# Performance work log

Measured on AMD Instinct MI355X. Metric: run time of the kernel, lower is better.

The kernel has to match this reference:

```python
import jax, jax.numpy as jnp
import numpy as np

B, S, D = 16, 8192, 256
CHUNK_RATIO = 4
EPS = 1e-8  # torch F.cosine_similarity default eps


def setup_inputs() -> dict:
    key = jax.random.key(0)
    ks = jax.random.split(key, 9)
    s = 1.0 / np.sqrt(D).astype(np.float32)
    return {
        "x": jax.random.normal(ks[0], (B, S, D), jnp.float32),
        "Wq": jax.random.normal(ks[1], (D, D), jnp.float32) * s,
        "bq": jax.random.normal(ks[2], (D,), jnp.float32) * s,
        "Wk": jax.random.normal(ks[3], (D, D), jnp.float32) * s,
        "bk": jax.random.normal(ks[4], (D,), jnp.float32) * s,
        "w_vol": jax.random.normal(ks[5], (D,), jnp.float32) * s,
        "b_vol": jax.random.normal(ks[6], (1,), jnp.float32) * s,
        "w_volu": jax.random.normal(ks[7], (D,), jnp.float32) * s,
        "b_volu": jax.random.normal(ks[8], (1,), jnp.float32) * s,
    }


def reference(x, Wq, bq, Wk, bk, w_vol, b_vol, w_volu, b_volu):
    Bn, Sn, Dn = x.shape
    q = x @ Wq + bq                       # (B,S,D)
    k = x @ Wk + bk                       # (B,S,D)
    qs, kx = q[:, 1:], k[:, :-1]          # (B,S-1,D)
    dot = jnp.sum(qs * kx, axis=-1)
    sim = dot / (jnp.maximum(jnp.linalg.norm(qs, axis=-1), EPS)
                 * jnp.maximum(jnp.linalg.norm(kx, axis=-1), EPS))
    boundary_scores = 1.0 - sim           # (B,S-1)
    vol = jax.nn.sigmoid(x @ w_vol + b_vol[0])     # (B,S)
    volu = jax.nn.sigmoid(x @ w_volu + b_volu[0])  # (B,S)
    combined = jnp.concatenate(
        [jnp.ones((Bn, 1), x.dtype),
         boundary_scores + 0.3 * vol[:, 1:] + 0.2 * volu[:, 1:]], axis=1)
    boundary_probs = jax.nn.sigmoid(combined)      # (B,S)
    hard = (boundary_probs > 0.5).astype(x.dtype)  # first pos always 1 (sigmoid(1)>0.5)
    boundaries = hard + boundary_probs - jax.lax.stop_gradient(boundary_probs)
    target = jnp.asarray(Sn / CHUNK_RATIO, x.dtype)
    ratio_loss = (boundaries.sum(axis=1).mean() - target) ** 2
    # vectorized compaction: gather boundary rows to the front, zero-pad to S
    idx = jnp.cumsum(hard.astype(jnp.int32), axis=1) - 1  # destination slot per row
    brow = jnp.arange(Bn)[:, None]
    compressed = jnp.zeros((Bn, Sn, Dn), x.dtype).at[brow, idx].add(x * hard[..., None])
    return compressed, boundary_probs, ratio_loss
```

## Files before the change

kernel.cpp:

```cpp
#include <hip/hip_runtime.h>
#include <math.h>

#define BN 16
#define SN 8192
#define DN 256
#define MBLK 128
#define EPSF 1e-8f

#define CHUNK_B 16384
#define NCHUNK 17
#define LDS_BYTES (3 * CHUNK_B)

typedef __attribute__((ext_vector_type(8))) short short8;
typedef __attribute__((ext_vector_type(4))) float f32x4;

typedef const __attribute__((address_space(1))) unsigned int g_u32;
typedef __attribute__((address_space(3))) unsigned int l_u32;

__device__ __forceinline__ unsigned short f2bf(float f) {
    union { float f; unsigned int u; } cv; cv.f = f;
    unsigned int u = cv.u + 0x7FFFu + ((cv.u >> 16) & 1u);
    return (unsigned short)(u >> 16);
}

__device__ __forceinline__ void gload_lds16(const void* g, void* l) {
    __builtin_amdgcn_global_load_lds((g_u32*)g, (l_u32*)l, 16, 0, 0);
}

__global__ void k0_prep(const float* __restrict__ Wq, const float* __restrict__ Wk,
                        const float* __restrict__ w_vol, const float* __restrict__ w_volu,
                        unsigned char* __restrict__ Wfrag)
{
    const int tid = threadIdx.x;
    const int n   = blockIdx.x * 8 + (tid >> 5);
    const int k8  = tid & 31;
    const int ch  = n >> 4;
    const int cc  = n & 15;
    const int ks  = k8 >> 2;
    const int g   = k8 & 3;

    short8 vq, vk;
    #pragma unroll
    for (int e = 0; e < 8; ++e) {
        const int k = k8 * 8 + e;
        vq[e] = (short)f2bf(Wq[(size_t)k * DN + n]);
        vk[e] = (short)f2bf(Wk[(size_t)k * DN + n]);
    }
    const size_t base = (size_t)ch * CHUNK_B + (size_t)((g * 16 + cc) * 16);
    *(short8*)(Wfrag + base + (size_t)(ks)     * 1024) = vq;
    *(short8*)(Wfrag + base + (size_t)(8 + ks) * 1024) = vk;

    unsigned char* Gfrag = Wfrag + (size_t)16 * CHUNK_B;
    if (blockIdx.x < 2) {
        const int gc = blockIdx.x * 8 + (tid >> 5);
        short8 vg;
        #pragma unroll
        for (int e = 0; e < 8; ++e) {
            const int k = k8 * 8 + e;
            float v = (gc == 0) ? w_vol[k] : ((gc == 1) ? w_volu[k] : 0.0f);
            vg[e] = (short)f2bf(v);
        }
        *(short8*)(Gfrag + (size_t)ks * 1024 + (size_t)((g * 16 + gc) * 16)) = vg;
    } else if (blockIdx.x < 4) {
        short8 z = (short8)(0);
        *(short8*)(Gfrag + 8192 + (size_t)(blockIdx.x - 2) * 4096 + (size_t)tid * 16) = z;
    }
}

__global__ void k0b_kpatch(const float* __restrict__ x, const float* __restrict__ Wk,
                           float* __restrict__ kpatch)
{
    __shared__ float xr[8][DN];
    const int b  = blockIdx.y;
    const int r0 = blockIdx.x * 8;
    const int t  = threadIdx.x;
    #pragma unroll
    for (int m = 0; m < 8; ++m)
        xr[m][t] = x[((size_t)b * SN + 31 + (size_t)(r0 + m) * 32) * DN + t];
    __syncthreads();
    float acc[8];
    #pragma unroll
    for (int m = 0; m < 8; ++m) acc[m] = 0.f;
    #pragma unroll 4
    for (int k = 0; k < DN; ++k) {
        const float w = Wk[(size_t)k * DN + t];
        #pragma unroll
        for (int m = 0; m < 8; ++m) acc[m] = fmaf(xr[m][k], w, acc[m]);
    }
    #pragma unroll
    for (int m = 0; m < 8; ++m)
        kpatch[((size_t)b * 256 + r0 + m) * DN + t] = acc[m];
}

__global__ __launch_bounds__(256, 3) void k1_mfma(
    const float* __restrict__ x,
    const unsigned char* __restrict__ Wfrag,
    const float* __restrict__ kpatch,
    const float* __restrict__ bq, const float* __restrict__ bk,
    const float* __restrict__ b_vol, const float* __restrict__ b_volu,
    float* __restrict__ bp_out, int* __restrict__ flags)
{
    extern __shared__ unsigned char lds[];

    const int tid  = threadIdx.x;
    const int wq   = tid >> 6;
    const int l    = tid & 63;
    const int g    = l >> 4;
    const int c    = l & 15;
    const int b    = blockIdx.y;
    const int blkx = blockIdx.x;
    const int s0   = blkx * MBLK;

    const float* xb = x + (size_t)b * SN * DN;

    {
        unsigned char* reg = lds;
        #pragma unroll
        for (int it = 0; it < 4; ++it) {
            const int f = it * 256 + tid;
            const int rho = f >> 5, ch = f & 31;
            const float4* p = (const float4*)(xb + (size_t)(s0 + rho) * DN + ch * 8);
            const float4 aa = p[0], dd = p[1];
            short8 sv;
            sv[0] = (short)f2bf(aa.x); sv[1] = (short)f2bf(aa.y);
            sv[2] = (short)f2bf(aa.z); sv[3] = (short)f2bf(aa.w);
            sv[4] = (short)f2bf(dd.x); sv[5] = (short)f2bf(dd.y);
            sv[6] = (short)f2bf(dd.z); sv[7] = (short)f2bf(dd.w);
            *(short8*)(reg + rho * 512 + ((ch * 16) ^ ((rho & 7) << 4))) = sv;
        }
    }
    __syncthreads();

    short8 a[2][8];
    #pragma unroll
    for (int qt = 0; qt < 4; ++qt) {
        if (qt < 3) {
            unsigned char* reg = lds + ((qt + 1) & 1) * CHUNK_B;
            #pragma unroll
            for (int it = 0; it < 4; ++it) {
                const int f = it * 256 + tid;
                const int rho = f >> 5, ch = f & 31;
                const float4* p = (const float4*)(xb + (size_t)(s0 + (qt + 1) * 32 + rho) * DN + ch * 8);
                const float4 aa = p[0], dd = p[1];
                short8 sv;
                sv[0] = (short)f2bf(aa.x); sv[1] = (short)f2bf(aa.y);
                sv[2] = (short)f2bf(aa.z); sv[3] = (short)f2bf(aa.w);
                sv[4] = (short)f2bf(dd.x); sv[5] = (short)f2bf(dd.y);
                sv[6] = (short)f2bf(dd.z); sv[7] = (short)f2bf(dd.w);
                *(short8*)(reg + rho * 512 + ((ch * 16) ^ ((rho & 7) << 4))) = sv;
            }
        }
        if (wq == qt) {
            const unsigned char* reg = lds + (qt & 1) * CHUNK_B;
            #pragma unroll
            for (int m = 0; m < 2; ++m) {
                const int rho = m * 16 + c;
                #pragma unroll
                for (int ks = 0; ks < 8; ++ks)
                    a[m][ks] = *(const short8*)(reg + rho * 512 + (((ks * 64) + g * 16) ^ ((rho & 7) << 4)));
            }
        }
        __syncthreads();
    }

    #pragma unroll
    for (int j = 0; j < 4; ++j)
        gload_lds16(Wfrag + j * 4096 + tid * 16, lds + j * 4096 + wq * 1024);
    #pragma unroll
    for (int j = 0; j < 4; ++j)
        gload_lds16(Wfrag + CHUNK_B + j * 4096 + tid * 16, lds + CHUNK_B + j * 4096 + wq * 1024);
    asm volatile("s_waitcnt vmcnt(4)" ::: "memory");
    __builtin_amdgcn_s_barrier();

    float dt[2][4], nqv[2][4], nkv[2][4];
    #pragma unroll
    for (int m = 0; m < 2; ++m)
        #pragma unroll
        for (int r = 0; r < 4; ++r) { dt[m][r] = 0.f; nqv[m][r] = 0.f; nkv[m][r] = 0.f; }
    f32x4 cg0 = (f32x4)(0.f), cg1 = (f32x4)(0.f);

    int kpidx = 4 * blkx + wq - 1;
    if (kpidx < 0) kpidx = 0;
    const float* kpp = kpatch + ((size_t)b * 256 + kpidx) * DN;

    #pragma unroll
    for (int i = 0; i < NCHUNK; ++i) {
        if (i + 2 < NCHUNK) {
            const unsigned char* src = Wfrag + (size_t)(i + 2) * CHUNK_B;
            unsigned char* dst = lds + ((i + 2) % 3) * CHUNK_B;
            #pragma unroll
            for (int j = 0; j < 4; ++j)
                gload_lds16(src + j * 4096 + tid * 16, dst + j * 4096 + wq * 1024);
        }
        const unsigned char* bb = lds + (i % 3) * CHUNK_B;

        if (i < 16) {
            f32x4 cq0 = (f32x4)(0.f), cq1 = (f32x4)(0.f);
            f32x4 ck0 = (f32x4)(0.f), ck1 = (f32x4)(0.f);
            #pragma unroll
            for (int ks = 0; ks < 8; ++ks) {
                const short8 bqf = *(const short8*)(bb + ks * 1024 + l * 16);
                const short8 bkf = *(const short8*)(bb + (8 + ks) * 1024 + l * 16);
                cq0 = __builtin_amdgcn_mfma_f32_16x16x32_bf16(a[0][ks], bqf, cq0, 0, 0, 0);
                cq1 = __builtin_amdgcn_mfma_f32_16x16x32_bf16(a[1][ks], bqf, cq1, 0, 0, 0);
                ck0 = __builtin_amdgcn_mfma_f32_16x16x32_bf16(a[0][ks], bkf, ck0, 0, 0, 0);
                ck1 = __builtin_amdgcn_mfma_f32_16x16x32_bf16(a[1][ks], bkf, ck1, 0, 0, 0);
            }
            const float bqc = bq[i * 16 + c];
            const float bkc = bk[i * 16 + c];
            const float kb  = kpp[i * 16 + c];
            const float sh0 = __shfl(ck0[3], (l - 16) & 63);
            const float sh1 = __shfl(ck1[3], (l - 16) & 63);
            const float cr  = __shfl(ck0[3], 48 + c);
            const float km00 = (g == 0) ? kb : sh0;
            const float km10 = (g == 0) ? cr : sh1;
            const float kv0[4] = {km00, ck0[0], ck0[1], ck0[2]};
            const float kv1[4] = {km10, ck1[0], ck1[1], ck1[2]};
            #pragma unroll
            for (int r = 0; r < 4; ++r) {
                float qv = cq0[r] + bqc;
                float kv = kv0[r] + bkc;
                dt[0][r]  = fmaf(qv, kv, dt[0][r]);
                nqv[0][r] = fmaf(qv, qv, nqv[0][r]);
                nkv[0][r] = fmaf(kv, kv, nkv[0][r]);
                qv = cq1[r] + bqc;
                kv = kv1[r] + bkc;
                dt[1][r]  = fmaf(qv, kv, dt[1][r]);
                nqv[1][r] = fmaf(qv, qv, nqv[1][r]);
                nkv[1][r] = fmaf(kv, kv, nkv[1][r]);
            }
        } else {
            #pragma unroll
            for (int ks = 0; ks < 8; ++ks) {
                const short8 bgf = *(const short8*)(bb + ks * 1024 + l * 16);
                cg0 = __builtin_amdgcn_mfma_f32_16x16x32_bf16(a[0][ks], bgf, cg0, 0, 0, 0);
                cg1 = __builtin_amdgcn_mfma_f32_16x16x32_bf16(a[1][ks], bgf, cg1, 0, 0, 0);
            }
        }

        if (i < NCHUNK - 2) asm volatile("s_waitcnt vmcnt(4)" ::: "memory");
        else                asm volatile("s_waitcnt vmcnt(0)" ::: "memory");
        __builtin_amdgcn_s_barrier();
    }

    #pragma unroll
    for (int m = 0; m < 2; ++m)
        #pragma unroll
        for (int r = 0; r < 4; ++r) {
            float aa = dt[m][r], e = nqv[m][r], f = nkv[m][r];
            #pragma unroll
            for (int mask = 1; mask < 16; mask <<= 1) {
                aa += __shfl_xor(aa, mask);
                e  += __shfl_xor(e, mask);
                f  += __shfl_xor(f, mask);
            }
            dt[m][r] = aa; nqv[m][r] = e; nkv[m][r] = f;
        }
    float vu0[4], vu1[4];
    #pragma unroll
    for (int r = 0; r < 4; ++r) { vu0[r] = __shfl_xor(cg0[r], 1); vu1[r] = __shfl_xor(cg1[r], 1); }

    if (c == 0) {
        const float bv = b_vol[0], bu = b_volu[0];
        #pragma unroll
        for (int m = 0; m < 2; ++m)
            #pragma unroll
            for (int r = 0; r < 4; ++r) {
                const int s = s0 + wq * 32 + m * 16 + g * 4 + r;
                const float cgv = (m == 0) ? cg0[r] : cg1[r];
                const float vuv = (m == 0) ? vu0[r] : vu1[r];
                float comb;
                if (s == 0) comb = 1.0f;
                else {
                    float denom = fmaxf(sqrtf(nqv[m][r]), EPSF) * fmaxf(sqrtf(nkv[m][r]), EPSF);
                    float sim   = dt[m][r] / denom;
                    float vol   = 1.f / (1.f + expf(-(cgv + bv)));
                    float volu  = 1.f / (1.f + expf(-(vuv + bu)));
                    comb = (1.f - sim) + 0.3f * vol + 0.2f * volu;
                }
                const float pbp = 1.f / (1.f + expf(-comb));
                const size_t o = (size_t)b * SN + s;
                bp_out[o] = pbp;
                flags[o]  = (pbp > 0.5f) ? 1 : 0;
            }
    }
}

__global__ void k2_scan(const int* __restrict__ flags,
                        const float* __restrict__ bp,
                        int* __restrict__ pidx,
                        int* __restrict__ cnt,
                        float* __restrict__ bsum)
{
    const int b = blockIdx.x;
    const int t = threadIdx.x;
    __shared__ int   ssum[256];
    __shared__ float sf[256];

    const size_t base = (size_t)b * SN + (size_t)t * 32;
    int f[32];
    int run = 0;
    float fs = 0.f;
    #pragma unroll
    for (int i = 0; i < 32; ++i) {
        f[i] = flags[base + i];
        run += f[i];
        float p  = bp[base + i];
        float hf = (float)f[i];
        fs += hf + p - p;
    }
    ssum[t] = run;
    sf[t]   = fs;
    __syncthreads();

    for (int off = 1; off < 256; off <<= 1) {
        int v = (t >= off) ? ssum[t - off] : 0;
        __syncthreads();
        ssum[t] += v;
        __syncthreads();
    }
    const int incl = ssum[t];
    int running = incl - run;
    #pragma unroll
    for (int i = 0; i < 32; ++i) {
        running += f[i];
        pidx[base + i] = f[i] ? (running - 1) : -1;
    }
    if (t == 255) cnt[b] = incl;

    for (int off = 128; off > 0; off >>= 1) {
        if (t < off) sf[t] += sf[t + off];
        __syncthreads();
    }
    if (t == 0) bsum[b] = sf[0];
}

__global__ void k3_scatter(const float* __restrict__ x,
                           const int* __restrict__ pidx,
                           float* __restrict__ out_comp)
{
    const int row  = blockIdx.x * 4 + (threadIdx.x >> 6);
    const int lane = threadIdx.x & 63;
    const int p = pidx[row];
    if (p < 0) return;
    const int b = row >> 13;
    const float4* src = (const float4*)(x + (size_t)row * DN);
    float4* dst = (float4*)(out_comp + ((size_t)b * SN + p) * DN);
    dst[lane] = src[lane];
}

__global__ void k3b_zerotail(float* __restrict__ out_comp,
                             const int* __restrict__ cnt)
{
    const int gid = blockIdx.x * blockDim.x + threadIdx.x;
    const int b = gid >> 13;
    const int j = gid & (SN - 1);
    if (j >= cnt[b]) {
        float4* dst = (float4*)(out_comp + ((size_t)b * SN + j) * DN);
        const float4 z = make_float4(0.f, 0.f, 0.f, 0.f);
        for (int i = 0; i < DN / 4; ++i) dst[i] = z;
    }
}

__global__ void k4_loss(const float* __restrict__ bsum, float* __restrict__ out_rl)
{
    if (threadIdx.x == 0) {
        float acc = 0.f;
        for (int i = 0; i < BN; ++i) acc += bsum[i];
        float mean = acc / (float)BN;
        float d = mean - (float)(SN / 4);
        out_rl[0] = d * d;
    }
}

extern "C" void kernel_launch(void* const* d_in, const int* in_sizes, int n_in,
                              void* d_out, int out_size, void* d_ws, size_t ws_size,
                              hipStream_t stream) {
    const float* x      = (const float*)d_in[0];
    const float* Wq     = (const float*)d_in[1];
    const float* bq     = (const float*)d_in[2];
    const float* Wk     = (const float*)d_in[3];
    const float* bk     = (const float*)d_in[4];
    const float* w_vol  = (const float*)d_in[5];
    const float* b_vol  = (const float*)d_in[6];
    const float* w_volu = (const float*)d_in[7];
    const float* b_volu = (const float*)d_in[8];

    float* out_comp = (float*)d_out;
    float* out_bp   = out_comp + (size_t)BN * SN * DN;
    float* out_rl   = out_bp + (size_t)BN * SN;

    int*   flags = (int*)d_ws;
    int*   pidx  = flags + (size_t)BN * SN;
    int*   cnt   = pidx + (size_t)BN * SN;
    float* bsum  = (float*)(cnt + BN);
    unsigned char* Wfrag = (unsigned char*)(bsum + BN);
    float* kpatch = (float*)(Wfrag + (size_t)NCHUNK * CHUNK_B);

    k0_prep<<<32, 256, 0, stream>>>(Wq, Wk, w_vol, w_volu, Wfrag);

    k0b_kpatch<<<dim3(32, BN), 256, 0, stream>>>(x, Wk, kpatch);

    hipFuncSetAttribute((const void*)k1_mfma,
                        hipFuncAttributeMaxDynamicSharedMemorySize, LDS_BYTES);

    k1_mfma<<<dim3(SN / MBLK, BN), 256, LDS_BYTES, stream>>>(
        x, Wfrag, kpatch, bq, bk, b_vol, b_volu, out_bp, flags);

    k2_scan<<<BN, 256, 0, stream>>>(flags, out_bp, pidx, cnt, bsum);

    k3_scatter<<<(BN * SN) / 4, 256, 0, stream>>>(x, pidx, out_comp);

    k3b_zerotail<<<(BN * SN) / 256, 256, 0, stream>>>(out_comp, cnt);

    k4_loss<<<1, 64, 0, stream>>>(bsum, out_rl);
}
```

Before: 139.4 us.

## Double k1 block to 512 threads and 256 rows with 4-stage weight pipeline

The main projection kernel now handles 256 rows per block with 8 waves instead of 128 rows with 4. Each staged weight chunk is therefore shared by twice as many waves, and the weight prefetch ring grows from 3 to 4 LDS buffers with a deeper wait schedule. MFMA sections are wrapped in s_setprio raises. The kpatch kernel is re-tiled to 16 rows per block with float4 LDS reads. The larger LDS footprint and bigger blocks may lower occupancy, and the rest of k1, which is not shown, has to handle 8 waves correctly.

```diff
diff --git a/kernel.cpp b/kernel.cpp
--- a/kernel.cpp
+++ b/kernel.cpp
@@ -4,12 +4,12 @@
 #define BN 16
 #define SN 8192
 #define DN 256
-#define MBLK 128
+#define MBLK 256
 #define EPSF 1e-8f
 
 #define CHUNK_B 16384
 #define NCHUNK 17
-#define LDS_BYTES (3 * CHUNK_B)
+#define LDS_BYTES (4 * CHUNK_B)
 
 typedef __attribute__((ext_vector_type(8))) short short8;
 typedef __attribute__((ext_vector_type(4))) float f32x4;
@@ -70,29 +70,35 @@
 __global__ void k0b_kpatch(const float* __restrict__ x, const float* __restrict__ Wk,
                            float* __restrict__ kpatch)
 {
-    __shared__ float xr[8][DN];
+    __shared__ float xr[16][DN];
     const int b  = blockIdx.y;
-    const int r0 = blockIdx.x * 8;
+    const int r0 = blockIdx.x * 16;
     const int t  = threadIdx.x;
     #pragma unroll
-    for (int m = 0; m < 8; ++m)
+    for (int m = 0; m < 16; ++m)
         xr[m][t] = x[((size_t)b * SN + 31 + (size_t)(r0 + m) * 32) * DN + t];
     __syncthreads();
-    float acc[8];
-    #pragma unroll
-    for (int m = 0; m < 8; ++m) acc[m] = 0.f;
-    #pragma unroll 4
-    for (int k = 0; k < DN; ++k) {
-        const float w = Wk[(size_t)k * DN + t];
-        #pragma unroll
-        for (int m = 0; m < 8; ++m) acc[m] = fmaf(xr[m][k], w, acc[m]);
-    }
-    #pragma unroll
-    for (int m = 0; m < 8; ++m)
+    float acc[16];
+    #pragma unroll
+    for (int m = 0; m < 16; ++m) acc[m] = 0.f;
+    #pragma unroll 2
+    for (int k = 0; k < DN; k += 4) {
+        const float w0 = Wk[(size_t)k * DN + t];
+        const float w1 = Wk[(size_t)(k + 1) * DN + t];
+        const float w2 = Wk[(size_t)(k + 2) * DN + t];
+        const float w3 = Wk[(size_t)(k + 3) * DN + t];
+        #pragma unroll
+        for (int m = 0; m < 16; ++m) {
+            const float4 xv = *(const float4*)&xr[m][k];
+            acc[m] = fmaf(xv.w, w3, fmaf(xv.z, w2, fmaf(xv.y, w1, fmaf(xv.x, w0, acc[m]))));
+        }
+    }
+    #pragma unroll
+    for (int m = 0; m < 16; ++m)
         kpatch[((size_t)b * 256 + r0 + m) * DN + t] = acc[m];
 }
 
-__global__ __launch_bounds__(256, 3) void k1_mfma(
+__global__ __launch_bounds__(512, 4) void k1_mfma(
     const float* __restrict__ x,
     const unsigned char* __restrict__ Wfrag,
     const float* __restrict__ kpatch,
@@ -113,62 +119,63 @@
 
     const float* xb = x + (size_t)b * SN * DN;
 
+    short8 a[2][8];
     {
-        unsigned char* reg = lds;
-        #pragma unroll
-        for (int it = 0; it < 4; ++it) {
-            const int f = it * 256 + tid;
-            const int rho = f >> 5, ch = f & 31;
-            const float4* p = (const float4*)(xb + (size_t)(s0 + rho) * DN + ch * 8);
-            const float4 aa = p[0], dd = p[1];
-            short8 sv;
-            sv[0] = (short)f2bf(aa.x); sv[1] = (short)f2bf(aa.y);
-            sv[2] = (short)f2bf(aa.z); sv[3] = (short)f2bf(aa.w);
-            sv[4] = (short)f2bf(dd.x); sv[5] = (short)f2bf(dd.y);
-            sv[6] = (short)f2bf(dd.z); sv[7] = (short)f2bf(dd.w);
-            *(short8*)(reg + rho * 512 + ((ch * 16) ^ ((rho & 7) << 4))) = sv;
-        }
-    }
-    __syncthreads();
-
-    short8 a[2][8];
-    #pragma unroll
-    for (int qt = 0; qt < 4; ++qt) {
-        if (qt < 3) {
-            unsigned char* reg = lds + ((qt + 1) & 1) * CHUNK_B;
+        {
+            unsigned char* reg = lds;
             #pragma unroll
             for (int it = 0; it < 4; ++it) {
-                const int f = it * 256 + tid;
-                const int rho = f >> 5, ch = f & 31;
-                const float4* p = (const float4*)(xb + (size_t)(s0 + (qt + 1) * 32 + rho) * DN + ch * 8);
+                const int f = it * 512 + tid;
+                const int lr = f >> 5, ch = f & 31;
+                const float4* p = (const float4*)(xb + (size_t)(s0 + lr) * DN + ch * 8);
                 const float4 aa = p[0], dd = p[1];
                 short8 sv;
                 sv[0] = (short)f2bf(aa.x); sv[1] = (short)f2bf(aa.y);
                 sv[2] = (short)f2bf(aa.z); sv[3] = (short)f2bf(aa.w);
                 sv[4] = (short)f2bf(dd.x); sv[5] = (short)f2bf(dd.y);
                 sv[6] = (short)f2bf(dd.z); sv[7] = (short)f2bf(dd.w);
-                *(short8*)(reg + rho * 512 + ((ch * 16) ^ ((rho & 7) << 4))) = sv;
-            }
-        }
-        if (wq == qt) {
-            const unsigned char* reg = lds + (qt & 1) * CHUNK_B;
-            #pragma unroll
-            for (int m = 0; m < 2; ++m) {
-                const int rho = m * 16 + c;
+                *(short8*)(reg + lr * 512 + ((ch * 16) ^ ((lr & 7) << 4))) = sv;
+            }
+        }
+        __syncthreads();
+        #pragma unroll
+        for (int j = 0; j < 4; ++j) {
+            if (j < 3) {
+                unsigned char* reg = lds + ((j + 1) & 1) * 32768;
                 #pragma unroll
-                for (int ks = 0; ks < 8; ++ks)
-                    a[m][ks] = *(const short8*)(reg + rho * 512 + (((ks * 64) + g * 16) ^ ((rho & 7) << 4)));
-            }
-        }
-        __syncthreads();
-    }
-
-    #pragma unroll
-    for (int j = 0; j < 4; ++j)
-        gload_lds16(Wfrag + j * 4096 + tid * 16, lds + j * 4096 + wq * 1024);
-    #pragma unroll
-    for (int j = 0; j < 4; ++j)
-        gload_lds16(Wfrag + CHUNK_B + j * 4096 + tid * 16, lds + CHUNK_B + j * 4096 + wq * 1024);
+                for (int it = 0; it < 4; ++it) {
+                    const int f = it * 512 + tid;
+                    const int lr = f >> 5, ch = f & 31;
+                    const float4* p = (const float4*)(xb + (size_t)(s0 + (j + 1) * 64 + lr) * DN + ch * 8);
+                    const float4 aa = p[0], dd = p[1];
+                    short8 sv;
+                    sv[0] = (short)f2bf(aa.x); sv[1] = (short)f2bf(aa.y);
+                    sv[2] = (short)f2bf(aa.z); sv[3] = (short)f2bf(aa.w);
+                    sv[4] = (short)f2bf(dd.x); sv[5] = (short)f2bf(dd.y);
+                    sv[6] = (short)f2bf(dd.z); sv[7] = (short)f2bf(dd.w);
+                    *(short8*)(reg + lr * 512 + ((ch * 16) ^ ((lr & 7) << 4))) = sv;
+                }
+            }
+            if ((wq >> 1) == j) {
+                const unsigned char* reg = lds + (j & 1) * 32768;
+                #pragma unroll
+                for (int m = 0; m < 2; ++m) {
+                    const int lr = (wq & 1) * 32 + m * 16 + c;
+                    #pragma unroll
+                    for (int ks = 0; ks < 8; ++ks)
+                        a[m][ks] = *(const short8*)(reg + lr * 512 + (((ks * 64) + g * 16) ^ ((lr & 7) << 4)));
+                }
+            }
+            __syncthreads();
+        }
+    }
+
+    #pragma unroll
+    for (int ch = 0; ch < 3; ++ch)
+        #pragma unroll
+        for (int jj = 0; jj < 2; ++jj)
+            gload_lds16(Wfrag + (size_t)ch * CHUNK_B + jj * 8192 + tid * 16,
+                        lds + ch * CHUNK_B + jj * 8192 + wq * 1024);
     asm volatile("s_waitcnt vmcnt(4)" ::: "memory");
     __builtin_amdgcn_s_barrier();
 
@@ -179,24 +186,24 @@
         for (int r = 0; r < 4; ++r) { dt[m][r] = 0.f; nqv[m][r] = 0.f; nkv[m][r] = 0.f; }
     f32x4 cg0 = (f32x4)(0.f), cg1 = (f32x4)(0.f);
 
-    int kpidx = 4 * blkx + wq - 1;
+    int kpidx = 8 * blkx + wq - 1;
     if (kpidx < 0) kpidx = 0;
     const float* kpp = kpatch + ((size_t)b * 256 + kpidx) * DN;
 
     #pragma unroll
     for (int i = 0; i < NCHUNK; ++i) {
-        if (i + 2 < NCHUNK) {
-            const unsigned char* src = Wfrag + (size_t)(i + 2) * CHUNK_B;
-            unsigned char* dst = lds + ((i + 2) % 3) * CHUNK_B;
-            #pragma unroll
-            for (int j = 0; j < 4; ++j)
-                gload_lds16(src + j * 4096 + tid * 16, dst + j * 4096 + wq * 1024);
-        }
-        const unsigned char* bb = lds + (i % 3) * CHUNK_B;
+        if (i + 3 < NCHUNK) {
+            #pragma unroll
+            for (int jj = 0; jj < 2; ++jj)
+                gload_lds16(Wfrag + (size_t)(i + 3) * CHUNK_B + jj * 8192 + tid * 16,
+                            lds + ((i + 3) & 3) * CHUNK_B + jj * 8192 + wq * 1024);
+        }
+        const unsigned char* bb = lds + (i & 3) * CHUNK_B;
 
         if (i < 16) {
             f32x4 cq0 = (f32x4)(0.f), cq1 = (f32x4)(0.f);
             f32x4 ck0 = (f32x4)(0.f), ck1 = (f32x4)(0.f);
+            __builtin_amdgcn_s_setprio(1);
             #pragma unroll
             for (int ks = 0; ks < 8; ++ks) {
                 const short8 bqf = *(const short8*)(bb + ks * 1024 + l * 16);
@@ -206,6 +213,7 @@
                 ck0 = __builtin_amdgcn_mfma_f32_16x16x32_bf16(a[0][ks], bkf, ck0, 0, 0, 0);
                 ck1 = __builtin_amdgcn_mfma_f32_16x16x32_bf16(a[1][ks], bkf, ck1, 0, 0, 0);
             }
+            __builtin_amdgcn_s_setprio(0);
             const float bqc = bq[i * 16 + c];
             const float bkc = bk[i * 16 + c];
             const float kb  = kpp[i * 16 + c];
@@ -230,16 +238,19 @@
                 nkv[1][r] = fmaf(kv, kv, nkv[1][r]);
             }
         } else {
+            __builtin_amdgcn_s_setprio(1);
             #pragma unroll
             for (int ks = 0; ks < 8; ++ks) {
                 const short8 bgf = *(const short8*)(bb + ks * 1024 + l * 16);
                 cg0 = __builtin_amdgcn_mfma_f32_16x16x32_bf16(a[0][ks], bgf, cg0, 0, 0, 0);
                 cg1 = __builtin_amdgcn_mfma_f32_16x16x32_bf16(a[1][ks], bgf, cg1, 0, 0, 0);
             }
-        }
-
-        if (i < NCHUNK - 2) asm volatile("s_waitcnt vmcnt(4)" ::: "memory");
-        else                asm volatile("s_waitcnt vmcnt(0)" ::: "memory");
+            __builtin_amdgcn_s_setprio(0);
+        }
+
+        if (i + 3 < NCHUNK)      asm volatile("s_waitcnt vmcnt(4)" ::: "memory");
+        else if (i + 2 < NCHUNK) asm volatile("s_waitcnt vmcnt(2)" ::: "memory");
+        else if (i + 1 < NCHUNK) asm volatile("s_waitcnt vmcnt(0)" ::: "memory");
         __builtin_amdgcn_s_barrier();
     }
 
@@ -399,12 +410,12 @@
 
     k0_prep<<<32, 256, 0, stream>>>(Wq, Wk, w_vol, w_volu, Wfrag);
 
-    k0b_kpatch<<<dim3(32, BN), 256, 0, stream>>>(x, Wk, kpatch);
+    k0b_kpatch<<<dim3(16, BN), 256, 0, stream>>>(x, Wk, kpatch);
 
     hipFuncSetAttribute((const void*)k1_mfma,
                         hipFuncAttributeMaxDynamicSharedMemorySize, LDS_BYTES);
 
-    k1_mfma<<<dim3(SN / MBLK, BN), 256, LDS_BYTES, stream>>>(
+    k1_mfma<<<dim3(SN / MBLK, BN), 512, LDS_BYTES, stream>>>(
         x, Wfrag, kpatch, bq, bk, b_vol, b_volu, out_bp, flags);
 
     k2_scan<<<BN, 256, 0, stream>>>(flags, out_bp, pidx, cnt, bsum);
```

Result: slower. 152.4 us (+9.4%).
